# Kernel tuning notes

Hardware: AMD Instinct MI355X
Metric: run time of the kernel (lower is better)

The kernel has to match this reference:

```python
import jax, jax.numpy as jnp
import numpy as np

B, N, IN, OUT, H = 16, 1024, 512, 512, 4

def setup_inputs() -> dict:
    key = jax.random.key(0)
    ks = jax.random.split(key, 10)
    s = 0.03  # small init scale to keep tanh/sigmoid in sane range
    return {
        "h": jax.random.normal(ks[0], (B, N, IN), jnp.float32),
        "adj": jax.random.randint(ks[1], (B, N, N), 0, 2) > 0,
        "W": jax.random.normal(ks[2], (H, OUT, IN), jnp.float32) * s,   # per-head Linear weight [out,in]
        "bW": jax.random.normal(ks[3], (H, OUT), jnp.float32) * s,
        "attn": jax.random.normal(ks[4], (H, OUT, OUT), jnp.float32) * s,
        "A_w": jax.random.normal(ks[5], (OUT, OUT * H), jnp.float32) * s,
        "fc_w": jax.random.normal(ks[6], (OUT, IN), jnp.float32) * s,
        "g1_w": jax.random.normal(ks[7], (OUT, OUT), jnp.float32) * s,
        "g2_w": jax.random.normal(ks[8], (OUT, OUT), jnp.float32) * s,
        "gbias": jax.random.normal(ks[9], (OUT,), jnp.float32) * s,
    }

def reference(h, adj, W, bW, attn, A_w, fc_w, g1_w, g2_w, gbias):
    # Per-head projection: Wh[b,h,n,o] = h @ W_h^T + b_h  (dropout is identity at inference)
    Wh = jnp.einsum('bni,hoi->bhno', h, W) + bW[None, :, None, :]
    # Bilinear attention scores: Wh @ attn_h @ Wh^T, masked by adjacency, then tanh
    e = jnp.einsum('bhno,hop->bhnp', Wh, attn)          # [B,H,N,O]
    scores = jnp.einsum('bhnp,bhmp->bhnm', e, Wh)       # [B,H,N,N]
    A_mat = jnp.tanh(jnp.where(adj[:, None, :, :], scores, 0.0))
    # Aggregate neighbors and relu
    hp = jax.nn.relu(jnp.einsum('bhnm,bhmo->bhno', A_mat, Wh))  # [B,H,N,O]
    # Concat heads (relu of relu is identity), project with A
    cat = jnp.transpose(hp, (0, 2, 1, 3)).reshape(hp.shape[0], hp.shape[2], -1)  # [B,N,H*O]
    ha = cat @ A_w.T                                     # [B,N,O]
    hf = h @ fc_w.T                                      # [B,N,O]
    # Sigmoid-gated fusion of the two branches
    coeff = jax.nn.sigmoid(hf @ g1_w.T + ha @ g2_w.T + gbias)
    return hf * coeff + ha * (1.0 - coeff)
```

## Files before the change

kernel.cpp:

```cpp
#include <hip/hip_runtime.h>
#include <hip/hip_fp16.h>


typedef _Float16 h8 __attribute__((ext_vector_type(8)));
typedef _Float16 h4 __attribute__((ext_vector_type(4)));
typedef float f4 __attribute__((ext_vector_type(4)));

__device__ __forceinline__ void load_lds16(const void* g, void* l) {
  __builtin_amdgcn_global_load_lds(
      (const __attribute__((address_space(1))) unsigned int*)g,
      (__attribute__((address_space(3))) unsigned int*)l, 16, 0, 0);
}

struct GP {
  const _Float16* A; const _Float16* B; void* C; const float* bias;
  const unsigned long long* adjb; const _Float16* gcat;
  int K, ldA, ldB, ldC, z0, ntx, nty, nz;
  long sAz, sAb, sBz, sBh, sCz, sCb, sCh, sBiasH;
};

__device__ __forceinline__ void stage_tiles(const _Float16* Ag, const _Float16* Bg,
                                            _Float16* As, _Float16* Bs,
                                            int ldA, int ldB, int wv, int rs, int cs) {
#pragma unroll
  for (int ps = 0; ps < 4; ++ps) {
    int c = ps * 4 + wv;
    int r = c * 8 + rs;
    int kb = (cs ^ (r & 7)) * 8;
    load_lds16(Ag + (long)r * ldA + kb, As + c * 512);
    load_lds16(Bg + (long)r * ldB + kb, Bs + c * 512);
  }
}

__device__ __forceinline__ void compute_tile(const _Float16* As, const _Float16* Bs,
                                             f4 acc[4][4], int wr, int wc, int l15, int lg) {
#pragma unroll
  for (int ks = 0; ks < 2; ++ks) {
    h8 av[4], bv[4];
    const int kby = ks * 64 + lg * 16;
#pragma unroll
    for (int m = 0; m < 4; ++m) {
      int row = wr * 64 + m * 16 + l15;
      av[m] = *(const h8*)((const char*)As + row * 128 + (kby ^ ((row & 7) << 4)));
    }
#pragma unroll
    for (int n = 0; n < 4; ++n) {
      int col = wc * 64 + n * 16 + l15;
      bv[n] = *(const h8*)((const char*)Bs + col * 128 + (kby ^ ((col & 7) << 4)));
    }
#pragma unroll
    for (int m = 0; m < 4; ++m)
#pragma unroll
      for (int n = 0; n < 4; ++n)
        acc[m][n] = __builtin_amdgcn_mfma_f32_16x16x32_f16(av[m], bv[n], acc[m][n], 0, 0, 0);
  }
}

template<int EPI>
__global__ __launch_bounds__(256) void gemm_bt(GP p) {
  __shared__ __align__(16) char smem[32768];
  _Float16* Ash = (_Float16*)smem;
  _Float16* Bsh = (_Float16*)(smem + 16384);
  _Float16* Cld = (_Float16*)smem;

  const int tid = threadIdx.x;
  const int wv = tid >> 6;
  const int ln = tid & 63;
  const int l15 = ln & 15;
  const int lg = ln >> 4;
  const int wr = wv >> 1, wc = wv & 1;
  const int rs = ln >> 3;
  const int cs = ln & 7;

  const int bid = blockIdx.x;
  const int ntile = p.ntx * p.nty;
  int zl, tx, ty;
  if (p.nz > 1) {
    int xcd = bid & 7;
    int u = bid >> 3;
    zl = xcd + 8 * (u / ntile);
    int t = u % ntile;
    tx = t % p.ntx;
    ty = t / p.ntx;
  } else {
    int xcd = bid & 7;
    int u = bid >> 3;
    int t = xcd * (ntile >> 3) + u;
    zl = 0;
    tx = t % p.ntx;
    ty = t / p.ntx;
  }
  const int zg = p.z0 + zl;
  const int bg = zg >> 2, hg = zg & 3;
  const _Float16* A = p.A + p.sAz * zl + p.sAb * bg;
  const _Float16* Bm = p.B + p.sBz * zl + p.sBh * hg;
  const long m0 = (long)tx * 128;
  const long n0 = (long)ty * 128;
  const int nk = p.K >> 6;

  f4 acc[4][4];
#pragma unroll
  for (int i = 0; i < 4; ++i)
#pragma unroll
    for (int j = 0; j < 4; ++j) acc[i][j] = (f4)(0.0f);

  const _Float16* Ag = A + m0 * p.ldA;
  const _Float16* Bg = Bm + n0 * p.ldB;

  for (int kt = 0; kt < nk; ++kt) {
    stage_tiles(Ag + kt * 64, Bg + kt * 64, Ash, Bsh, p.ldA, p.ldB, wv, rs, cs);
    __syncthreads();
    compute_tile(Ash, Bsh, acc, wr, wc, l15, lg);
    __syncthreads();
  }

  const long coff = p.sCz * zl + p.sCb * bg + p.sCh * hg;
  const float* bias = p.bias ? (p.bias + p.sBiasH * hg) : nullptr;
#pragma unroll
  for (int m = 0; m < 4; ++m) {
#pragma unroll
    for (int j = 0; j < 4; ++j) {
      int lrow = wr * 64 + m * 16 + lg * 4 + j;
      long grow = m0 + lrow;
      int vx = (lrow & 12) << 2;
      unsigned long long w;
      if (EPI == 2)
        w = p.adjb[(long)bg * 16384 + grow * 16 + (n0 >> 6) + wc];
#pragma unroll
      for (int n = 0; n < 4; ++n) {
        int lcol = wc * 64 + n * 16 + l15;
        float v = acc[m][n][j];
        if (EPI == 1 || EPI == 5) v += bias[n0 + lcol];
        if (EPI == 2) {
          if ((w >> (n * 16 + l15)) & 1ull) {
            float ex = __expf(2.0f * v);
            v = 1.0f - 2.0f * __builtin_amdgcn_rcpf(ex + 1.0f);
          } else v = 0.0f;
        }
        if (EPI == 3) v = v > 0.0f ? v : 0.0f;
        if (EPI == 5) v = __builtin_amdgcn_rcpf(1.0f + __expf(-v));
        Cld[lrow * 128 + (lcol ^ vx)] = (_Float16)v;
      }
    }
  }
  __syncthreads();
  if (EPI == 5) {
    float* C = (float*)p.C;
#pragma unroll
    for (int it = 0; it < 8; ++it) {
      int row = it * 16 + (tid >> 4);
      int col0 = (tid & 15) * 8;
      int vx = (row & 12) << 2;
      h8 cfv = *(const h8*)&Cld[row * 128 + (col0 ^ vx)];
      long grow = m0 + row;
      long gc = n0 + col0;
      h8 hfv = *(const h8*)&p.gcat[grow * 1024 + gc];
      h8 hav = *(const h8*)&p.gcat[grow * 1024 + 512 + gc];
      float o[8];
#pragma unroll
      for (int j = 0; j < 8; ++j) {
        float cf = (float)cfv[j];
        o[j] = (float)hfv[j] * cf + (float)hav[j] * (1.0f - cf);
      }
      float* op = &C[coff + grow * p.ldC + gc];
      *(float4*)op = make_float4(o[0], o[1], o[2], o[3]);
      *(float4*)(op + 4) = make_float4(o[4], o[5], o[6], o[7]);
    }
  } else {
    _Float16* C = (_Float16*)p.C;
#pragma unroll
    for (int it = 0; it < 8; ++it) {
      int row = it * 16 + (tid >> 4);
      int col0 = (tid & 15) * 8;
      int vx = (row & 12) << 2;
      h8 o = *(const h8*)&Cld[row * 128 + (col0 ^ vx)];
      *(h8*)&C[coff + (m0 + row) * p.ldC + n0 + col0] = o;
    }
  }
}

__global__ __launch_bounds__(256) void trans_h16(const _Float16* in, _Float16* out) {
  __shared__ _Float16 tl[64][72];
  const long zi = blockIdx.z;
  const _Float16* I = in + zi * 524288;
  _Float16* O = out + zi * 524288;
  const int r0 = blockIdx.x * 64, c0 = blockIdx.y * 64;
  const int t = threadIdx.x;
  const int rr = t >> 3, c8 = (t & 7) * 8;
#pragma unroll
  for (int it = 0; it < 2; ++it) {
    int r = rr + it * 32;
    h8 v = *(const h8*)&I[(long)(r0 + r) * 512 + c0 + c8];
#pragma unroll
    for (int j = 0; j < 8; ++j) tl[c8 + j][r] = v[j];
  }
  __syncthreads();
#pragma unroll
  for (int it = 0; it < 2; ++it) {
    int c = rr + it * 32;
    h8 w;
#pragma unroll
    for (int j = 0; j < 8; ++j) w[j] = tl[c][c8 + j];
    *(h8*)&O[(long)(c0 + c) * 1024 + r0 + c8] = w;
  }
}

__global__ void trans_attn(const float* attn, _Float16* attnT) {
  __shared__ _Float16 tl[64][65];
  const long hh = blockIdx.z;
  const float* I = attn + hh * 262144;
  _Float16* O = attnT + hh * 262144;
  const int r0 = blockIdx.x * 64, c0 = blockIdx.y * 64;
  for (int i = threadIdx.x; i < 4096; i += 256) {
    int r = i >> 6, c = i & 63;
    tl[c][r] = (_Float16)I[(long)(r0 + r) * 512 + c0 + c];
  }
  __syncthreads();
  for (int i = threadIdx.x; i < 4096; i += 256) {
    int c = i >> 6, r = i & 63;
    O[(long)(c0 + c) * 512 + r0 + r] = tl[c][r];
  }
}

__global__ void cvt_f16(const float* in, _Float16* out, int n4) {
  int i = blockIdx.x * 256 + threadIdx.x;
  if (i < n4) {
    float4 v = ((const float4*)in)[i];
    h4 o = {(_Float16)v.x, (_Float16)v.y, (_Float16)v.z, (_Float16)v.w};
    ((h4*)out)[i] = o;
  }
}

__global__ void build_gw(const float* g1, const float* g2, _Float16* gw) {
  int i = blockIdx.x * 256 + threadIdx.x;
  int o = i >> 10, k = i & 1023;
  float v = (k < 512) ? g1[o * 512 + k] : g2[o * 512 + (k - 512)];
  gw[i] = (_Float16)v;
}

__global__ void detect_fmt(const unsigned char* adj, int* flags) {
  __shared__ int sa, sb, sc;
  if (threadIdx.x == 0) { sa = 0; sb = 0; sc = 0; }
  __syncthreads();
  int a = 0, b = 0, c = 0;
  for (int i = threadIdx.x; i < 4096; i += 256) {
    if (adj[i]) {
      if (i & 3) a = 1;
      else c = 1;
      if ((i & 7) == 4) b = 1;
    }
  }
  if (a) sa = 1;
  if (b) sb = 1;
  if (c) sc = 1;
  __syncthreads();
  if (threadIdx.x == 0) {
    int fmt;
    if (sa) fmt = sc ? 1 : 3;
    else fmt = sb ? 0 : 2;
    flags[0] = fmt;
  }
}

__global__ void adj_bits(const void* adj, const int* flags, unsigned long long* adjb) {
  long i = (long)blockIdx.x * 256 + threadIdx.x;
  int fmt = flags[0];
  bool v;
  if (fmt == 1) v = ((const unsigned char*)adj)[i] != 0;
  else if (fmt == 3) v = ((const float*)adj)[i] != 0.0f;
  else if (fmt == 2) v = ((const long long*)adj)[i] != 0;
  else v = ((const int*)adj)[i] != 0;
  unsigned long long m = __ballot(v);
  if ((threadIdx.x & 63) == 0) adjb[i >> 6] = m;
}

extern "C" void kernel_launch(void* const* d_in, const int* in_sizes, int n_in,
                              void* d_out, int out_size, void* d_ws, size_t ws_size,
                              hipStream_t stream) {
  const float* h    = (const float*)d_in[0];
  const void*  adj  = d_in[1];
  const float* W    = (const float*)d_in[2];
  const float* bW   = (const float*)d_in[3];
  const float* attn = (const float*)d_in[4];
  const float* A_w  = (const float*)d_in[5];
  const float* fc_w = (const float*)d_in[6];
  const float* g1   = (const float*)d_in[7];
  const float* g2   = (const float*)d_in[8];
  const float* gbias= (const float*)d_in[9];
  float* out = (float*)d_out;
  char* ws = (char*)d_ws;
  (void)in_sizes; (void)n_in; (void)out_size;

  const size_t MB = 1ull << 20;
  const size_t fixedB = 96 * MB;
  int ZCv = 16;
  if (fixedB + 5 * 32 * MB + 8 * MB <= ws_size) ZCv = 32;
  if (fixedB + 5 * 64 * MB + 8 * MB <= ws_size) ZCv = 64;
  const int nchunk = 64 / ZCv;

  size_t off = 0;
  auto alloc = [&](size_t sz) { size_t o = off; off += (sz + 255) & ~(size_t)255; return o; };
  const size_t oFlags = alloc(256);
  const size_t oH16   = alloc(16 * MB);
  const size_t oW16   = alloc(2 * MB);
  const size_t oAttnT = alloc(2 * MB);
  const size_t oAw16  = alloc(2 * MB);
  const size_t oFc16  = alloc(512 * 1024);
  const size_t oGw16  = alloc(1 * MB);
  const size_t oAdjb  = alloc(2 * MB);
  const size_t oCat   = alloc(64 * MB);
  const size_t oWhC   = alloc((size_t)ZCv * MB);
  const size_t oEC    = alloc((size_t)ZCv * MB);
  const size_t oWhTC  = alloc((size_t)ZCv * MB);
  const size_t oAmatC = alloc((size_t)ZCv * 2 * MB);
  const size_t oGcat  = oWhC;
  (void)ws_size;

  int* flags = (int*)(ws + oFlags);
  _Float16* h16   = (_Float16*)(ws + oH16);
  _Float16* W16   = (_Float16*)(ws + oW16);
  _Float16* attnT = (_Float16*)(ws + oAttnT);
  _Float16* Aw16  = (_Float16*)(ws + oAw16);
  _Float16* fc16  = (_Float16*)(ws + oFc16);
  _Float16* gw16  = (_Float16*)(ws + oGw16);
  unsigned long long* adjb = (unsigned long long*)(ws + oAdjb);
  _Float16* cat   = (_Float16*)(ws + oCat);
  _Float16* WhC   = (_Float16*)(ws + oWhC);
  _Float16* eC    = (_Float16*)(ws + oEC);
  _Float16* WhTC  = (_Float16*)(ws + oWhTC);
  _Float16* AmatC = (_Float16*)(ws + oAmatC);
  _Float16* gcat  = (_Float16*)(ws + oGcat);

  detect_fmt<<<1, 256, 0, stream>>>((const unsigned char*)adj, flags);
  adj_bits<<<65536, 256, 0, stream>>>(adj, flags, adjb);
  cvt_f16<<<8192, 256, 0, stream>>>(h, h16, 2097152);
  cvt_f16<<<1024, 256, 0, stream>>>(W, W16, 262144);
  cvt_f16<<<1024, 256, 0, stream>>>(A_w, Aw16, 262144);
  cvt_f16<<<256, 256, 0, stream>>>(fc_w, fc16, 65536);
  build_gw<<<2048, 256, 0, stream>>>(g1, g2, gw16);
  trans_attn<<<dim3(8, 8, 4), 256, 0, stream>>>(attn, attnT);

  for (int c = 0; c < nchunk; ++c) {
    const int z0 = c * ZCv;
    GP q;
    q = GP{};
    q.A = h16; q.B = W16; q.C = WhC; q.bias = bW;
    q.K = 512; q.ldA = 512; q.ldB = 512; q.ldC = 512; q.z0 = z0;
    q.ntx = 8; q.nty = 4; q.nz = ZCv;
    q.sAz = 0; q.sAb = 524288; q.sBz = 0; q.sBh = 262144;
    q.sCz = 524288; q.sCb = 0; q.sCh = 0; q.sBiasH = 512;
    gemm_bt<1><<<32 * ZCv, 256, 0, stream>>>(q);
    q = GP{};
    q.A = WhC; q.B = attnT; q.C = eC;
    q.K = 512; q.ldA = 512; q.ldB = 512; q.ldC = 512; q.z0 = z0;
    q.ntx = 8; q.nty = 4; q.nz = ZCv;
    q.sAz = 524288; q.sBh = 262144; q.sCz = 524288;
    gemm_bt<0><<<32 * ZCv, 256, 0, stream>>>(q);
    trans_h16<<<dim3(16, 8, ZCv), 256, 0, stream>>>(WhC, WhTC);
    q = GP{};
    q.A = eC; q.B = WhC; q.C = AmatC; q.adjb = adjb;
    q.K = 512; q.ldA = 512; q.ldB = 512; q.ldC = 1024; q.z0 = z0;
    q.ntx = 8; q.nty = 8; q.nz = ZCv;
    q.sAz = 524288; q.sBz = 524288; q.sCz = 1048576;
    gemm_bt<2><<<64 * ZCv, 256, 0, stream>>>(q);
    q = GP{};
    q.A = AmatC; q.B = WhTC; q.C = cat;
    q.K = 1024; q.ldA = 1024; q.ldB = 1024; q.ldC = 2048; q.z0 = z0;
    q.sAz = 1048576; q.sBz = 524288;
    q.ntx = 8; q.nty = 4; q.nz = ZCv;
    q.sCz = 0; q.sCb = 2097152; q.sCh = 512;
    gemm_bt<3><<<32 * ZCv, 256, 0, stream>>>(q);
  }

  GP q;
  q = GP{};
  q.A = h16; q.B = fc16; q.C = gcat;
  q.K = 512; q.ldA = 512; q.ldB = 512; q.ldC = 1024; q.z0 = 0;
  q.ntx = 128; q.nty = 4; q.nz = 1;
  gemm_bt<0><<<512, 256, 0, stream>>>(q);
  q = GP{};
  q.A = cat; q.B = Aw16; q.C = gcat + 512;
  q.K = 2048; q.ldA = 2048; q.ldB = 2048; q.ldC = 1024; q.z0 = 0;
  q.ntx = 128; q.nty = 4; q.nz = 1;
  gemm_bt<0><<<512, 256, 0, stream>>>(q);
  q = GP{};
  q.A = gcat; q.B = gw16; q.C = out; q.bias = gbias; q.gcat = gcat;
  q.K = 1024; q.ldA = 1024; q.ldB = 1024; q.ldC = 512; q.z0 = 0;
  q.ntx = 128; q.nty = 4; q.nz = 1; q.sBiasH = 0;
  gemm_bt<5><<<512, 256, 0, stream>>>(q);
}
```

Measured before the change: 593.1 us.

## Fuse Wh transpose into projection GEMM epilogue and split gate mixing into separate kernel

```diff
diff --git a/kernel.cpp b/kernel.cpp
--- a/kernel.cpp
+++ b/kernel.cpp
@@ -14,9 +14,9 @@
 
 struct GP {
   const _Float16* A; const _Float16* B; void* C; const float* bias;
-  const unsigned long long* adjb; const _Float16* gcat;
+  const unsigned long long* adjb; _Float16* aux;
   int K, ldA, ldB, ldC, z0, ntx, nty, nz;
-  long sAz, sAb, sBz, sBh, sCz, sCb, sCh, sBiasH;
+  long sAz, sAb, sBz, sBh, sCz, sCb, sCh, sBiasH, sAuxZ;
 };
 
 __device__ __forceinline__ void stage_tiles(const _Float16* Ag, const _Float16* Bg,
@@ -57,7 +57,7 @@
 }
 
 template<int EPI>
-__global__ __launch_bounds__(256) void gemm_bt(GP p) {
+__device__ __forceinline__ void gemm_core(GP p) {
   __shared__ __align__(16) char smem[32768];
   _Float16* Ash = (_Float16*)smem;
   _Float16* Bsh = (_Float16*)(smem + 16384);
@@ -130,7 +130,7 @@
       for (int n = 0; n < 4; ++n) {
         int lcol = wc * 64 + n * 16 + l15;
         float v = acc[m][n][j];
-        if (EPI == 1 || EPI == 5) v += bias[n0 + lcol];
+        if (EPI == 5 || EPI == 6) v += bias[n0 + lcol];
         if (EPI == 2) {
           if ((w >> (n * 16 + l15)) & 1ull) {
             float ex = __expf(2.0f * v);
@@ -144,29 +144,7 @@
     }
   }
   __syncthreads();
-  if (EPI == 5) {
-    float* C = (float*)p.C;
-#pragma unroll
-    for (int it = 0; it < 8; ++it) {
-      int row = it * 16 + (tid >> 4);
-      int col0 = (tid & 15) * 8;
-      int vx = (row & 12) << 2;
-      h8 cfv = *(const h8*)&Cld[row * 128 + (col0 ^ vx)];
-      long grow = m0 + row;
-      long gc = n0 + col0;
-      h8 hfv = *(const h8*)&p.gcat[grow * 1024 + gc];
-      h8 hav = *(const h8*)&p.gcat[grow * 1024 + 512 + gc];
-      float o[8];
-#pragma unroll
-      for (int j = 0; j < 8; ++j) {
-        float cf = (float)cfv[j];
-        o[j] = (float)hfv[j] * cf + (float)hav[j] * (1.0f - cf);
-      }
-      float* op = &C[coff + grow * p.ldC + gc];
-      *(float4*)op = make_float4(o[0], o[1], o[2], o[3]);
-      *(float4*)(op + 4) = make_float4(o[4], o[5], o[6], o[7]);
-    }
-  } else {
+  {
     _Float16* C = (_Float16*)p.C;
 #pragma unroll
     for (int it = 0; it < 8; ++it) {
@@ -177,31 +155,50 @@
       *(h8*)&C[coff + (m0 + row) * p.ldC + n0 + col0] = o;
     }
   }
-}
-
-__global__ __launch_bounds__(256) void trans_h16(const _Float16* in, _Float16* out) {
-  __shared__ _Float16 tl[64][72];
-  const long zi = blockIdx.z;
-  const _Float16* I = in + zi * 524288;
-  _Float16* O = out + zi * 524288;
-  const int r0 = blockIdx.x * 64, c0 = blockIdx.y * 64;
-  const int t = threadIdx.x;
-  const int rr = t >> 3, c8 = (t & 7) * 8;
-#pragma unroll
-  for (int it = 0; it < 2; ++it) {
-    int r = rr + it * 32;
-    h8 v = *(const h8*)&I[(long)(r0 + r) * 512 + c0 + c8];
-#pragma unroll
-    for (int j = 0; j < 8; ++j) tl[c8 + j][r] = v[j];
-  }
-  __syncthreads();
-#pragma unroll
-  for (int it = 0; it < 2; ++it) {
-    int c = rr + it * 32;
-    h8 w;
-#pragma unroll
-    for (int j = 0; j < 8; ++j) w[j] = tl[c][c8 + j];
-    *(h8*)&O[(long)(c0 + c) * 1024 + r0 + c8] = w;
+  if (EPI == 6) {
+    _Float16* X = p.aux + p.sAuxZ * zl;
+#pragma unroll
+    for (int pass = 0; pass < 8; ++pass) {
+      int ol = pass * 16 + (tid >> 4);
+      int ml = (tid & 15) * 8;
+      h8 o;
+#pragma unroll
+      for (int j = 0; j < 8; ++j) {
+        int mm = ml + j;
+        o[j] = Cld[mm * 128 + (ol ^ ((mm & 12) << 2))];
+      }
+      *(h8*)&X[(n0 + ol) * 1024 + m0 + ml] = o;
+    }
+  }
+}
+
+#define GEMM_WRAP(name, epi) \
+  __global__ __launch_bounds__(256) void name(GP p) { gemm_core<epi>(p); }
+GEMM_WRAP(gemm_wh, 6)
+GEMM_WRAP(gemm_e, 0)
+GEMM_WRAP(gemm_amat, 2)
+GEMM_WRAP(gemm_cat, 3)
+GEMM_WRAP(gemm_hf, 0)
+GEMM_WRAP(gemm_ha, 0)
+GEMM_WRAP(gemm_gate, 5)
+
+__global__ __launch_bounds__(256) void mix_kernel(const _Float16* gcat,
+                                                  const _Float16* coeff, float* out) {
+  const int stride = gridDim.x * 256;
+  for (int g = blockIdx.x * 256 + threadIdx.x; g < 1048576; g += stride) {
+    int r = g >> 6, c8 = (g & 63) << 3;
+    h8 hf = *(const h8*)&gcat[(long)r * 1024 + c8];
+    h8 ha = *(const h8*)&gcat[(long)r * 1024 + 512 + c8];
+    h8 cf = *(const h8*)&coeff[(long)r * 512 + c8];
+    float o[8];
+#pragma unroll
+    for (int j = 0; j < 8; ++j) {
+      float c = (float)cf[j];
+      o[j] = (float)hf[j] * c + (float)ha[j] * (1.0f - c);
+    }
+    float* op = &out[(long)r * 512 + c8];
+    *(float4*)op = make_float4(o[0], o[1], o[2], o[3]);
+    *(float4*)(op + 4) = make_float4(o[4], o[5], o[6], o[7]);
   }
 }
 
@@ -292,10 +289,10 @@
   (void)in_sizes; (void)n_in; (void)out_size;
 
   const size_t MB = 1ull << 20;
-  const size_t fixedB = 96 * MB;
+  const size_t fixedB = 92 * MB;
   int ZCv = 16;
-  if (fixedB + 5 * 32 * MB + 8 * MB <= ws_size) ZCv = 32;
-  if (fixedB + 5 * 64 * MB + 8 * MB <= ws_size) ZCv = 64;
+  if (fixedB + 5ull * 64 * MB <= ws_size) ZCv = 64;
+  else if (fixedB + 5ull * 32 * MB <= ws_size) ZCv = 32;
   const int nchunk = 64 / ZCv;
 
   size_t off = 0;
@@ -314,7 +311,7 @@
   const size_t oWhTC  = alloc((size_t)ZCv * MB);
   const size_t oAmatC = alloc((size_t)ZCv * 2 * MB);
   const size_t oGcat  = oWhC;
-  (void)ws_size;
+  const size_t oCoeff = oAmatC;
 
   int* flags = (int*)(ws + oFlags);
   _Float16* h16   = (_Float16*)(ws + oH16);
@@ -330,6 +327,7 @@
   _Float16* WhTC  = (_Float16*)(ws + oWhTC);
   _Float16* AmatC = (_Float16*)(ws + oAmatC);
   _Float16* gcat  = (_Float16*)(ws + oGcat);
+  _Float16* coeff = (_Float16*)(ws + oCoeff);
 
   detect_fmt<<<1, 256, 0, stream>>>((const unsigned char*)adj, flags);
   adj_bits<<<65536, 256, 0, stream>>>(adj, flags, adjb);
@@ -344,32 +342,31 @@
     const int z0 = c * ZCv;
     GP q;
     q = GP{};
-    q.A = h16; q.B = W16; q.C = WhC; q.bias = bW;
+    q.A = h16; q.B = W16; q.C = WhC; q.bias = bW; q.aux = WhTC;
     q.K = 512; q.ldA = 512; q.ldB = 512; q.ldC = 512; q.z0 = z0;
     q.ntx = 8; q.nty = 4; q.nz = ZCv;
     q.sAz = 0; q.sAb = 524288; q.sBz = 0; q.sBh = 262144;
-    q.sCz = 524288; q.sCb = 0; q.sCh = 0; q.sBiasH = 512;
-    gemm_bt<1><<<32 * ZCv, 256, 0, stream>>>(q);
+    q.sCz = 524288; q.sCb = 0; q.sCh = 0; q.sBiasH = 512; q.sAuxZ = 524288;
+    gemm_wh<<<32 * ZCv, 256, 0, stream>>>(q);
     q = GP{};
     q.A = WhC; q.B = attnT; q.C = eC;
     q.K = 512; q.ldA = 512; q.ldB = 512; q.ldC = 512; q.z0 = z0;
     q.ntx = 8; q.nty = 4; q.nz = ZCv;
     q.sAz = 524288; q.sBh = 262144; q.sCz = 524288;
-    gemm_bt<0><<<32 * ZCv, 256, 0, stream>>>(q);
-    trans_h16<<<dim3(16, 8, ZCv), 256, 0, stream>>>(WhC, WhTC);
+    gemm_e<<<32 * ZCv, 256, 0, stream>>>(q);
     q = GP{};
     q.A = eC; q.B = WhC; q.C = AmatC; q.adjb = adjb;
     q.K = 512; q.ldA = 512; q.ldB = 512; q.ldC = 1024; q.z0 = z0;
     q.ntx = 8; q.nty = 8; q.nz = ZCv;
     q.sAz = 524288; q.sBz = 524288; q.sCz = 1048576;
-    gemm_bt<2><<<64 * ZCv, 256, 0, stream>>>(q);
+    gemm_amat<<<64 * ZCv, 256, 0, stream>>>(q);
     q = GP{};
     q.A = AmatC; q.B = WhTC; q.C = cat;
     q.K = 1024; q.ldA = 1024; q.ldB = 1024; q.ldC = 2048; q.z0 = z0;
     q.sAz = 1048576; q.sBz = 524288;
     q.ntx = 8; q.nty = 4; q.nz = ZCv;
     q.sCz = 0; q.sCb = 2097152; q.sCh = 512;
-    gemm_bt<3><<<32 * ZCv, 256, 0, stream>>>(q);
+    gemm_cat<<<32 * ZCv, 256, 0, stream>>>(q);
   }
 
   GP q;
@@ -377,15 +374,16 @@
   q.A = h16; q.B = fc16; q.C = gcat;
   q.K = 512; q.ldA = 512; q.ldB = 512; q.ldC = 1024; q.z0 = 0;
   q.ntx = 128; q.nty = 4; q.nz = 1;
-  gemm_bt<0><<<512, 256, 0, stream>>>(q);
+  gemm_hf<<<512, 256, 0, stream>>>(q);
   q = GP{};
   q.A = cat; q.B = Aw16; q.C = gcat + 512;
   q.K = 2048; q.ldA = 2048; q.ldB = 2048; q.ldC = 1024; q.z0 = 0;
   q.ntx = 128; q.nty = 4; q.nz = 1;
-  gemm_bt<0><<<512, 256, 0, stream>>>(q);
+  gemm_ha<<<512, 256, 0, stream>>>(q);
   q = GP{};
-  q.A = gcat; q.B = gw16; q.C = out; q.bias = gbias; q.gcat = gcat;
+  q.A = gcat; q.B = gw16; q.C = coeff; q.bias = gbias;
   q.K = 1024; q.ldA = 1024; q.ldB = 1024; q.ldC = 512; q.z0 = 0;
   q.ntx = 128; q.nty = 4; q.nz = 1; q.sBiasH = 0;
-  gemm_bt<5><<<512, 256, 0, stream>>>(q);
-}
+  gemm_gate<<<512, 256, 0, stream>>>(q);
+  mix_kernel<<<2048, 256, 0, stream>>>(gcat, coeff, out);
+}
```

Result: faster. 526.9 us (-11.2%).
